# Kernel optimization log

Measured on AMD Instinct MI355X. Metric: run time of the kernel, lower is better.

Reference implementation:

```python
import jax, jax.numpy as jnp
import numpy as np

B, K, D, H, A = 8192, 10, 64, 128, 16
E = K * (K - 1)
# lexicographic ordered pairs (i,j), i != j -- matches adj.nonzero() and sorted(Dict.keys())
_PAIRS = np.array([(i, j) for i in range(K) for j in range(K) if i != j], dtype=np.int32)
SRC = jnp.asarray(_PAIRS[:, 0])  # message for edge (i,j) is aggregated at node i (row)
DST = jnp.asarray(_PAIRS[:, 1])


def setup_inputs() -> dict:
    key = jax.random.key(0)
    k1, k2, k3, k4, k5, k6 = jax.random.split(key, 6)
    F = D + H + A  # node MLP input dim
    return {
        "states": jax.random.normal(k1, (B, K, D), jnp.float32),
        "action_vec": jax.random.normal(k2, (B, K, A), jnp.float32),
        # one Linear(2D -> H) per ordered pair, stacked [E, 2D, H]
        "W_edge": jax.random.normal(k3, (E, 2 * D, H), jnp.float32) * (1.0 / np.sqrt(2 * D)),
        "b_edge": jax.random.normal(k4, (E, H), jnp.float32) * 0.01,
        # one Linear(D+H+A -> D) per node, stacked [K, F, D]
        "W_node": jax.random.normal(k5, (K, F, D), jnp.float32) * (1.0 / np.sqrt(F)),
        "b_node": jax.random.normal(k6, (K, D), jnp.float32) * 0.01,
    }


def reference(states, action_vec, W_edge, b_edge, W_node, b_node):
    # states: [B,K,D], action_vec: [B,K,A]
    b, k, d = states.shape
    # gather endpoints per ordered edge: [B,E,2D]
    pair_feat = jnp.concatenate([states[:, SRC, :], states[:, DST, :]], axis=-1)
    # per-edge-type Linear + tanh, batched as one grouped GEMM: [B,E,H]
    msg = jnp.tanh(jnp.einsum('bef,efh->beh', pair_feat, W_edge) + b_edge)
    # unsorted_segment_sum over source node index (row): [B,K,H]
    agg = jnp.zeros((b, k, msg.shape[-1]), msg.dtype).at[:, SRC, :].add(msg)
    # node input: [x, action, agg] -> per-node Linear + tanh: [B,K,D]
    node_in = jnp.concatenate([states, action_vec, agg], axis=-1)
    out = jnp.tanh(jnp.einsum('bkf,kfd->bkd', node_in, W_node) + b_node)
    return out
```

## Files before the change

### kernel.cpp

```cpp
#include <hip/hip_runtime.h>

typedef _Float16 f16;
typedef _Float16 f16x4 __attribute__((ext_vector_type(4)));
typedef _Float16 f16x8 __attribute__((ext_vector_type(8)));
typedef float    f32x4 __attribute__((ext_vector_type(4)));

#define S2C 2.88539008177792681472f

#define OFF_STF  0u
#define OFF_AC   5242880u
#define OFF_WEF  6553600u
#define OFF_WNF  8028160u
#define OFF_BE2  8171520u
#define OFF_Z    8195840u

__device__ __forceinline__ float fast_exp2(float x){
#if __has_builtin(__builtin_amdgcn_exp2f)
    return __builtin_amdgcn_exp2f(x);
#else
    return exp2f(x);
#endif
}
__device__ __forceinline__ float fast_rcp(float x){
#if __has_builtin(__builtin_amdgcn_rcpf)
    return __builtin_amdgcn_rcpf(x);
#else
    return 1.0f/x;
#endif
}

#define MFMA16(a,b,c) __builtin_amdgcn_mfma_f32_16x16x32_f16(a,b,c,0,0,0)

__global__ void prep(const float* __restrict__ st, const float* __restrict__ ac,
                     const float* __restrict__ We, const float* __restrict__ be,
                     const float* __restrict__ Wn, const float* __restrict__ bn,
                     f16* __restrict__ ws16){
    const int bid = blockIdx.x, t = threadIdx.x;
    if (bid < 2560){
        int g = bid*256 + t;
        int lane = g&63, ks = (g>>6)&1, rt = (g>>7)&1, rg2 = (g>>8)&255, node = g>>16;
        int row = rg2*32 + rt*16 + (lane&15);
        int k   = ks*32 + (lane>>4)*8;
        const float* src = st + ((size_t)row*10 + node)*64 + k;
        const float4 v0 = *(const float4*)src;
        const float4 v1 = *(const float4*)(src+4);
        f16x8 h; h[0]=(f16)v0.x; h[1]=(f16)v0.y; h[2]=(f16)v0.z; h[3]=(f16)v0.w;
                 h[4]=(f16)v1.x; h[5]=(f16)v1.y; h[6]=(f16)v1.z; h[7]=(f16)v1.w;
        *(f16x8*)(ws16 + OFF_STF + (size_t)g*8) = h;
    } else if (bid < 3840){
        int g = (bid-2560)*256 + t;
        const float4 v = ((const float4*)ac)[g];
        f16x4 h; h[0]=(f16)v.x; h[1]=(f16)v.y; h[2]=(f16)v.z; h[3]=(f16)v.w;
        *(f16x4*)(ws16 + OFF_AC + (size_t)g*4) = h;
    } else if (bid < 4560){
        int g = (bid-3840)*256 + t;
        int l = g & 15, q = (g>>4)&3, cg = (g>>6)&7, ks = (g>>9)&3, e = g>>11;
        const float* src = We + e*16384 + (ks*32 + q*8)*128 + cg*16 + l;
        f16x8 h;
        #pragma unroll
        for (int u=0;u<8;u++) h[u] = (f16)src[u*128];
        *(f16x8*)(ws16 + OFF_WEF + (size_t)g*8) = h;
    } else if (bid < 4630){
        int g = (bid-4560)*256 + t;
        if (g < 17920){
            int l = g&15, q=(g>>4)&3, c=(g>>6)&3, r=g>>8;
            int ks2 = r % 7, kn = r / 7;
            f16x8 h;
            #pragma unroll
            for (int u=0;u<8;u++){
                int knew = ks2*32 + q*8 + u;
                int f = (knew < 128) ? (knew + 80) : (knew - 128);
                h[u] = (knew < 208) ? (f16)Wn[kn*13312 + f*64 + c*16 + l] : (f16)0.0f;
            }
            *(f16x8*)(ws16 + OFF_WNF + (size_t)kn*14336 + ((size_t)(ks2*4+c)*64 + q*16 + l)*8) = h;
        }
    } else {
        int g = (bid-4630)*256 + t;
        float* be2 = (float*)(ws16 + OFF_BE2);
        if (g < 11520)      be2[g] = S2C*be[g];
        else if (g < 12160) be2[g] = S2C*bn[g-11520];
        else if (g < 12168) ws16[OFF_Z + (g-12160)] = (f16)0.0f;
    }
}

__launch_bounds__(128, 2)
__global__ void gnn_main(const f16* __restrict__ ws16, float* __restrict__ out){
    __shared__ alignas(16) f16 sAgg[32*128];

    const f16* stf = ws16 + OFF_STF;
    const f16* Wef = ws16 + OFF_WEF;
    const float* be2 = (const float*)(ws16 + OFF_BE2);
    const float* bn2 = be2 + 11520;

    const int t = threadIdx.x, lane = t&63, wid = t>>6;
    const int l15 = lane&15, q = lane>>4, qo = q<<3;
    const int i  = blockIdx.x >> 8;
    const int rb = blockIdx.x & 255;
    const int b0 = rb*32;
    const int cs = wid;
    const int e0 = 9*i;

    f16x8 ajb[2][4];
    f16x8 bfb[2][4][4];

    {
        const int j0 = (i==0) ? 1 : 0;
        const f16* p = stf + (size_t)(j0*256 + rb)*2048 + lane*8;
        #pragma unroll
        for (int r=0; r<4; ++r) ajb[0][r] = *(const f16x8*)(p + r*512);
        const f16* wb = Wef + (size_t)(e0*32 + cs*4)*512 + lane*8;
        #pragma unroll
        for (int ks4=0; ks4<4; ++ks4)
            #pragma unroll
            for (int c=0; c<4; ++c)
                bfb[0][ks4][c] = *(const f16x8*)(wb + (ks4*8 + c)*512);
    }
    f16x8 ai[4];
    {
        const f16* p = stf + (size_t)(i*256 + rb)*2048 + lane*8;
        ai[0] = *(const f16x8*)p;        ai[1] = *(const f16x8*)(p+512);
        ai[2] = *(const f16x8*)(p+1024); ai[3] = *(const f16x8*)(p+1536);
    }

    f32x4 agg[2][4] = {};

    #pragma unroll
    for (int e=0; e<9; ++e){
        const int cur = e&1, nxt = cur^1;
        const int ebase = e0 + e;

        if (e < 8){
            const int j2 = (e+1) + ((e+1) >= i);
            const f16* p = stf + (size_t)(j2*256 + rb)*2048 + lane*8;
            #pragma unroll
            for (int r=0; r<4; ++r) ajb[nxt][r] = *(const f16x8*)(p + r*512);
            const f16* wb = Wef + (size_t)((ebase+1)*32 + cs*4)*512 + lane*8;
            #pragma unroll
            for (int ks4=0; ks4<4; ++ks4)
                #pragma unroll
                for (int c=0; c<4; ++c)
                    bfb[nxt][ks4][c] = *(const f16x8*)(wb + (ks4*8 + c)*512);
        }
        float bv[4];
        #pragma unroll
        for (int c=0; c<4; ++c) bv[c] = be2[ebase*128 + cs*64 + c*16 + l15];

        #pragma unroll
        for (int rt=0; rt<2; ++rt){
            f32x4 msg[4] = {};
            #pragma unroll
            for (int ks4=0; ks4<4; ++ks4){
                f16x8 a = (ks4 < 2) ? ai[rt*2 + ks4] : ajb[cur][rt*2 + (ks4-2)];
                #pragma unroll
                for (int c=0; c<4; ++c)
                    msg[c] = MFMA16(a, bfb[cur][ks4][c], msg[c]);
            }
            #pragma unroll
            for (int c=0; c<4; ++c)
                #pragma unroll
                for (int r2=0; r2<4; ++r2){
                    float tt = __builtin_fmaf(msg[c][r2], S2C, bv[c]);
                    float rr = fast_rcp(fast_exp2(tt) + 1.0f);
                    agg[rt][c][r2] = __builtin_fmaf(-2.0f, rr, agg[rt][c][r2]);
                }
        }
    }

    #pragma unroll
    for (int rt=0; rt<2; ++rt)
        #pragma unroll
        for (int c=0; c<4; ++c)
            #pragma unroll
            for (int r2=0; r2<4; ++r2){
                int lrow = rt*16 + q*4 + r2;
                int col  = cs*64 + c*16 + l15;
                sAgg[lrow*128 + (((col>>3) ^ (lrow&7))<<3) + (col&7)] = (f16)(agg[rt][c][r2] + 9.0f);
            }
    __syncthreads();

    f32x4 acc[4] = {};
    const f16* wnb = ws16 + OFF_WNF + (size_t)i*14336;
    const f16* acp = ws16 + OFF_AC;
    const f16* zb  = ws16 + OFF_Z;
    #pragma unroll
    for (int ks2=0; ks2<7; ++ks2){
        f16x8 a;
        if (ks2 < 4){
            int lrow = wid*16 + l15;
            a = *(const f16x8*)(sAgg + lrow*128 + (((ks2*4 + q) ^ (l15&7))<<3));
        } else if (ks2 < 6){
            a = *(const f16x8*)(stf + (size_t)(i*256 + rb)*2048 + wid*1024 + (ks2-4)*512 + lane*8);
        } else {
            int row = b0 + wid*16 + l15;
            const f16* ap = (q < 2) ? (acp + ((size_t)row*10 + i)*16 + qo) : zb;
            a = *(const f16x8*)ap;
        }
        f16x8 bf[4];
        #pragma unroll
        for (int c=0; c<4; ++c)
            bf[c] = *(const f16x8*)(wnb + (size_t)(ks2*4+c)*512 + lane*8);
        #pragma unroll
        for (int c=0; c<4; ++c)
            acc[c] = MFMA16(a, bf[c], acc[c]);
    }
    float bnv[4];
    #pragma unroll
    for (int c=0; c<4; ++c) bnv[c] = bn2[i*64 + c*16 + l15];
    #pragma unroll
    for (int c=0; c<4; ++c)
        #pragma unroll
        for (int r2=0; r2<4; ++r2){
            int row = b0 + wid*16 + q*4 + r2;
            int col = c*16 + l15;
            float tt = __builtin_fmaf(acc[c][r2], S2C, bnv[c]);
            float rr = fast_rcp(fast_exp2(tt) + 1.0f);
            out[((size_t)row*10 + i)*64 + col] = __builtin_fmaf(-2.0f, rr, 1.0f);
        }
}

extern "C" void kernel_launch(void* const* d_in, const int* in_sizes, int n_in,
                              void* d_out, int out_size, void* d_ws, size_t ws_size,
                              hipStream_t stream) {
    const float* states = (const float*)d_in[0];
    const float* action = (const float*)d_in[1];
    const float* W_edge = (const float*)d_in[2];
    const float* b_edge = (const float*)d_in[3];
    const float* W_node = (const float*)d_in[4];
    const float* b_node = (const float*)d_in[5];
    f16* ws16 = (f16*)d_ws;

    hipLaunchKernelGGL(prep, dim3(4678), dim3(256), 0, stream,
                       states, action, W_edge, b_edge, W_node, b_node, ws16);
    hipLaunchKernelGGL(gnn_main, dim3(2560), dim3(128), 0, stream,
                       ws16, (float*)d_out);
}
```

Measured before the change: 137.8 us.

## Stage edge weights in double-buffered LDS shared by 8 waves per block

Blocks grow from 2 to 8 waves and cover 128 batch rows. Each edge's weight tile is loaded cooperatively into a double-buffered shared-memory buffer and reused by four row groups, instead of every wave holding its own copy in registers. The node-MLP weights are prefetched into shared memory during the last edge iteration, and block IDs are swizzled so neighbouring blocks work on different nodes. This cuts global weight traffic and register pressure, at the cost of LDS reads inside the MFMA loop and a barrier on every edge iteration.

```diff
diff --git a/kernel.cpp b/kernel.cpp
--- a/kernel.cpp
+++ b/kernel.cpp
@@ -83,9 +83,9 @@
     }
 }
 
-__launch_bounds__(128, 2)
+__launch_bounds__(512, 4)
 __global__ void gnn_main(const f16* __restrict__ ws16, float* __restrict__ out){
-    __shared__ alignas(16) f16 sAgg[32*128];
+    __shared__ alignas(16) f16 sW[2][16384];
 
     const f16* stf = ws16 + OFF_STF;
     const f16* Wef = ws16 + OFF_WEF;
@@ -94,33 +94,37 @@
 
     const int t = threadIdx.x, lane = t&63, wid = t>>6;
     const int l15 = lane&15, q = lane>>4, qo = q<<3;
-    const int i  = blockIdx.x >> 8;
-    const int rb = blockIdx.x & 255;
-    const int b0 = rb*32;
-    const int cs = wid;
-    const int e0 = 9*i;
-
-    f16x8 ajb[2][4];
-    f16x8 bfb[2][4][4];
+    const int rg = wid>>1, cs = wid&1;
+
+    const int swz = (blockIdx.x & 7)*80 + (blockIdx.x >> 3);
+    const int rb  = swz / 10;
+    const int i   = swz - rb*10;
+    const int e0  = 9*i;
+    const int rbrow = rb*4 + rg;
 
     {
-        const int j0 = (i==0) ? 1 : 0;
-        const f16* p = stf + (size_t)(j0*256 + rb)*2048 + lane*8;
-        #pragma unroll
-        for (int r=0; r<4; ++r) ajb[0][r] = *(const f16x8*)(p + r*512);
-        const f16* wb = Wef + (size_t)(e0*32 + cs*4)*512 + lane*8;
-        #pragma unroll
-        for (int ks4=0; ks4<4; ++ks4)
-            #pragma unroll
-            for (int c=0; c<4; ++c)
-                bfb[0][ks4][c] = *(const f16x8*)(wb + (ks4*8 + c)*512);
-    }
-    f16x8 ai[4];
+        const f16* wsrc = Wef + (size_t)e0*16384 + (size_t)(wid*4)*512 + (size_t)lane*8;
+        f16x8 w0 = *(const f16x8*)(wsrc);
+        f16x8 w1 = *(const f16x8*)(wsrc+512);
+        f16x8 w2 = *(const f16x8*)(wsrc+1024);
+        f16x8 w3 = *(const f16x8*)(wsrc+1536);
+        f16* dst = &sW[0][wid*4*512 + lane*8];
+        *(f16x8*)(dst)      = w0;
+        *(f16x8*)(dst+512)  = w1;
+        *(f16x8*)(dst+1024) = w2;
+        *(f16x8*)(dst+1536) = w3;
+    }
+    f16x8 ai[4], ajb[2][4];
     {
-        const f16* p = stf + (size_t)(i*256 + rb)*2048 + lane*8;
+        const f16* p = stf + ((size_t)i*256 + rbrow)*2048 + lane*8;
         ai[0] = *(const f16x8*)p;        ai[1] = *(const f16x8*)(p+512);
         ai[2] = *(const f16x8*)(p+1024); ai[3] = *(const f16x8*)(p+1536);
-    }
+        const int j0 = (i==0) ? 1 : 0;
+        const f16* pj = stf + ((size_t)j0*256 + rbrow)*2048 + lane*8;
+        ajb[0][0] = *(const f16x8*)pj;        ajb[0][1] = *(const f16x8*)(pj+512);
+        ajb[0][2] = *(const f16x8*)(pj+1024); ajb[0][3] = *(const f16x8*)(pj+1536);
+    }
+    __syncthreads();
 
     f32x4 agg[2][4] = {};
 
@@ -129,22 +133,35 @@
         const int cur = e&1, nxt = cur^1;
         const int ebase = e0 + e;
 
+        f16x8 st0, st1, st2, st3;
+        if (e < 8){
+            const f16* wsrc = Wef + (size_t)(ebase+1)*16384 + (size_t)(wid*4)*512 + (size_t)lane*8;
+            st0 = *(const f16x8*)(wsrc);
+            st1 = *(const f16x8*)(wsrc+512);
+            st2 = *(const f16x8*)(wsrc+1024);
+            st3 = *(const f16x8*)(wsrc+1536);
+        } else {
+            const f16* wnf = ws16 + OFF_WNF + (size_t)i*14336 + wid*512 + lane*8;
+            st0 = *(const f16x8*)(wnf);
+            st1 = *(const f16x8*)(wnf + 8*512);
+            st2 = *(const f16x8*)(wnf + 16*512);
+            if (wid < 4) st3 = *(const f16x8*)(wnf + 24*512);
+        }
+
         if (e < 8){
             const int j2 = (e+1) + ((e+1) >= i);
-            const f16* p = stf + (size_t)(j2*256 + rb)*2048 + lane*8;
-            #pragma unroll
-            for (int r=0; r<4; ++r) ajb[nxt][r] = *(const f16x8*)(p + r*512);
-            const f16* wb = Wef + (size_t)((ebase+1)*32 + cs*4)*512 + lane*8;
-            #pragma unroll
-            for (int ks4=0; ks4<4; ++ks4)
-                #pragma unroll
-                for (int c=0; c<4; ++c)
-                    bfb[nxt][ks4][c] = *(const f16x8*)(wb + (ks4*8 + c)*512);
-        }
+            const f16* pj = stf + ((size_t)j2*256 + rbrow)*2048 + lane*8;
+            ajb[nxt][0] = *(const f16x8*)pj;
+            ajb[nxt][1] = *(const f16x8*)(pj+512);
+            ajb[nxt][2] = *(const f16x8*)(pj+1024);
+            ajb[nxt][3] = *(const f16x8*)(pj+1536);
+        }
+
         float bv[4];
         #pragma unroll
         for (int c=0; c<4; ++c) bv[c] = be2[ebase*128 + cs*64 + c*16 + l15];
 
+        const f16* wb = &sW[cur][cs*4*512 + lane*8];
         #pragma unroll
         for (int rt=0; rt<2; ++rt){
             f32x4 msg[4] = {};
@@ -152,8 +169,10 @@
             for (int ks4=0; ks4<4; ++ks4){
                 f16x8 a = (ks4 < 2) ? ai[rt*2 + ks4] : ajb[cur][rt*2 + (ks4-2)];
                 #pragma unroll
-                for (int c=0; c<4; ++c)
-                    msg[c] = MFMA16(a, bfb[cur][ks4][c], msg[c]);
+                for (int c=0; c<4; ++c){
+                    f16x8 b = *(const f16x8*)(wb + (ks4*8 + c)*512);
+                    msg[c] = MFMA16(a, b, msg[c]);
+                }
             }
             #pragma unroll
             for (int c=0; c<4; ++c)
@@ -164,44 +183,61 @@
                     agg[rt][c][r2] = __builtin_fmaf(-2.0f, rr, agg[rt][c][r2]);
                 }
         }
-    }
-
-    #pragma unroll
-    for (int rt=0; rt<2; ++rt)
-        #pragma unroll
-        for (int c=0; c<4; ++c)
-            #pragma unroll
-            for (int r2=0; r2<4; ++r2){
-                int lrow = rt*16 + q*4 + r2;
-                int col  = cs*64 + c*16 + l15;
-                sAgg[lrow*128 + (((col>>3) ^ (lrow&7))<<3) + (col&7)] = (f16)(agg[rt][c][r2] + 9.0f);
-            }
+
+        if (e < 8){
+            f16* dst = &sW[nxt][wid*4*512 + lane*8];
+            *(f16x8*)(dst)      = st0;
+            *(f16x8*)(dst+512)  = st1;
+            *(f16x8*)(dst+1024) = st2;
+            *(f16x8*)(dst+1536) = st3;
+        } else {
+            f16* dst = &sW[1][wid*512 + lane*8];
+            *(f16x8*)(dst)        = st0;
+            *(f16x8*)(dst+8*512)  = st1;
+            *(f16x8*)(dst+16*512) = st2;
+            if (wid < 4) *(f16x8*)(dst+24*512) = st3;
+        }
+        __syncthreads();
+    }
+
+    {
+        f16* sAgg = &sW[0][0];
+        #pragma unroll
+        for (int rt=0; rt<2; ++rt)
+            #pragma unroll
+            for (int c=0; c<4; ++c)
+                #pragma unroll
+                for (int r2=0; r2<4; ++r2){
+                    int lrow = rg*32 + rt*16 + q*4 + r2;
+                    int col  = cs*64 + c*16 + l15;
+                    sAgg[lrow*128 + (((col>>3) ^ (lrow&7))<<3) + (col&7)] = (f16)(agg[rt][c][r2] + 9.0f);
+                }
+    }
     __syncthreads();
 
     f32x4 acc[4] = {};
-    const f16* wnb = ws16 + OFF_WNF + (size_t)i*14336;
     const f16* acp = ws16 + OFF_AC;
     const f16* zb  = ws16 + OFF_Z;
+    const int b0 = rb*128;
     #pragma unroll
     for (int ks2=0; ks2<7; ++ks2){
         f16x8 a;
         if (ks2 < 4){
             int lrow = wid*16 + l15;
-            a = *(const f16x8*)(sAgg + lrow*128 + (((ks2*4 + q) ^ (l15&7))<<3));
+            a = *(const f16x8*)(&sW[0][lrow*128 + (((ks2*4 + q) ^ (l15&7))<<3)]);
         } else if (ks2 < 6){
-            a = *(const f16x8*)(stf + (size_t)(i*256 + rb)*2048 + wid*1024 + (ks2-4)*512 + lane*8);
+            a = *(const f16x8*)(stf + ((size_t)i*256 + rb*4 + (wid>>1))*2048
+                                + (wid&1)*1024 + (ks2-4)*512 + lane*8);
         } else {
             int row = b0 + wid*16 + l15;
             const f16* ap = (q < 2) ? (acp + ((size_t)row*10 + i)*16 + qo) : zb;
             a = *(const f16x8*)ap;
         }
-        f16x8 bf[4];
-        #pragma unroll
-        for (int c=0; c<4; ++c)
-            bf[c] = *(const f16x8*)(wnb + (size_t)(ks2*4+c)*512 + lane*8);
-        #pragma unroll
-        for (int c=0; c<4; ++c)
-            acc[c] = MFMA16(a, bf[c], acc[c]);
+        #pragma unroll
+        for (int c=0; c<4; ++c){
+            f16x8 bf = *(const f16x8*)(&sW[1][(ks2*4+c)*512 + lane*8]);
+            acc[c] = MFMA16(a, bf, acc[c]);
+        }
     }
     float bnv[4];
     #pragma unroll
@@ -231,6 +267,6 @@
 
     hipLaunchKernelGGL(prep, dim3(4678), dim3(256), 0, stream,
                        states, action, W_edge, b_edge, W_node, b_node, ws16);
-    hipLaunchKernelGGL(gnn_main, dim3(2560), dim3(128), 0, stream,
+    hipLaunchKernelGGL(gnn_main, dim3(640), dim3(512), 0, stream,
                        ws16, (float*)d_out);
 }
```

Measured after the change: 392.3 us. 2.85x slower.
